# Kernel tuning notes

Measured on AMD Instinct MI355X. Metric: run time of the kernel, lower is better.

Reference implementation:

```python
import jax, jax.numpy as jnp
import numpy as np
import math

B, H, W, CV = 8, 128, 128, 256
T, CT = 77, 512
HEADS, HEAD_DIM = 8, 32
TOP_M = 5
LN_EPS = 1e-5
NORM_EPS = 1e-6
CLAMP = 2.0


def _ln(x, w, b):
    mu = jnp.mean(x, axis=-1, keepdims=True)
    var = jnp.mean(jnp.square(x - mu), axis=-1, keepdims=True)
    return (x - mu) * jax.lax.rsqrt(var + LN_EPS) * w + b


def _l2norm(x):
    n = jnp.sqrt(jnp.sum(jnp.square(x), axis=-1, keepdims=True))
    return x / jnp.maximum(n, NORM_EPS)


def setup_inputs() -> dict:
    key = jax.random.key(0)
    ks = jax.random.split(key, 12)
    s = 0.02
    return {
        "visual_features": jax.random.normal(ks[0], (B, H, W, CV), jnp.float32),
        "text_features": jax.random.normal(ks[1], (B, T, CT), jnp.float32),
        "norm1_w": jnp.ones((CV,), jnp.float32),
        "norm1_b": jnp.zeros((CV,), jnp.float32),
        "q_w": s * jax.random.normal(ks[2], (CV, CV), jnp.float32),
        "q_b": jnp.zeros((CV,), jnp.float32),
        "k_w": s * jax.random.normal(ks[3], (CT, CV), jnp.float32),
        "k_b": jnp.zeros((CV,), jnp.float32),
        "v_w": s * jax.random.normal(ks[4], (CT, CV), jnp.float32),
        "v_b": jnp.zeros((CV,), jnp.float32),
        "out_w": s * jax.random.normal(ks[5], (CV, CV), jnp.float32),
        "out_b": jnp.zeros((CV,), jnp.float32),
        "gate_w": s * jax.random.normal(ks[6], (CV, 1), jnp.float32),
        "gate_b": jnp.zeros((1,), jnp.float32),
        "logit_scale": jnp.asarray(math.log(1.0 / 0.07), jnp.float32),
        "alpha": jnp.asarray(0.1, jnp.float32),
        "norm2_w": jnp.ones((CV,), jnp.float32),
        "norm2_b": jnp.zeros((CV,), jnp.float32),
        "ffn1_w": s * jax.random.normal(ks[7], (CV, 4 * CV), jnp.float32),
        "ffn1_b": jnp.zeros((4 * CV,), jnp.float32),
        "ffn2_w": s * jax.random.normal(ks[8], (4 * CV, CV), jnp.float32),
        "ffn2_b": jnp.zeros((CV,), jnp.float32),
    }


def reference(visual_features, text_features, norm1_w, norm1_b, q_w, q_b, k_w, k_b,
              v_w, v_b, out_w, out_b, gate_w, gate_b, logit_scale, alpha,
              norm2_w, norm2_b, ffn1_w, ffn1_b, ffn2_w, ffn2_b):
    b, h, w, cv = visual_features.shape
    n = h * w
    # Pre-LN then flatten spatial dims: (B, N, Cv)
    x = _ln(visual_features, norm1_w, norm1_b).reshape(b, n, cv)
    q_full = x @ q_w + q_b                      # (B, N, Cv)
    k_full = text_features @ k_w + k_b          # (B, T, Cv)
    v_full = text_features @ v_w + v_b          # (B, T, Cv)
    # padding mask: all-zero text tokens
    pad = jnp.sum(jnp.abs(text_features), axis=-1) <= 1e-6  # (B, T)
    # cosine-normalize over FULL Cv dim, then split heads
    q = _l2norm(q_full).reshape(b, n, HEADS, HEAD_DIM)
    k = _l2norm(k_full).reshape(b, -1, HEADS, HEAD_DIM)
    v = v_full.reshape(b, -1, HEADS, HEAD_DIM)
    scale = jnp.exp(jnp.clip(logit_scale, -CLAMP, CLAMP)) / jnp.sqrt(jnp.float32(HEAD_DIM))
    sim = jnp.einsum('bnhd,bthd->bnht', q, k) * scale  # (B, N, Hh, T)
    sim = jnp.where(pad[:, None, None, :], -jnp.inf, sim)
    # top-k pruning over text tokens (threshold at k-th value; ties measure-zero)
    topv = jax.lax.top_k(sim, TOP_M)[0]
    sim = jnp.where(sim >= topv[..., -1:], sim, -jnp.inf)
    attn = jax.nn.softmax(sim, axis=-1)
    aligned = jnp.einsum('bnht,bthd->bnhd', attn, v).reshape(b, n, cv)
    aligned = aligned @ out_w + out_b
    gate = jax.nn.sigmoid(x @ gate_w + gate_b)  # (B, N, 1)
    y = x + alpha * gate * aligned
    y = _ln(y, norm2_w, norm2_b)
    ffn = jax.nn.gelu(y @ ffn1_w + ffn1_b, approximate=False) @ ffn2_w + ffn2_b
    y = y + ffn
    return y.reshape(b, h, w, cv)
```

## Files before the change

### kernel.cpp

```cpp
#include <hip/hip_runtime.h>
#include <hip/hip_bf16.h>

typedef _Float16 h16;
typedef __attribute__((ext_vector_type(8))) _Float16 halfx8;
typedef __attribute__((ext_vector_type(4))) _Float16 halfx4;
typedef __attribute__((ext_vector_type(4))) float f32x4;

__device__ __forceinline__ void gload_lds16(const void* g, void* l) {
  __builtin_amdgcn_global_load_lds((const __attribute__((address_space(1))) unsigned int*)g,
                                   (__attribute__((address_space(3))) unsigned int*)l, 16, 0, 0);
}
__device__ __forceinline__ unsigned umax_(unsigned a, unsigned b) { return a > b ? a : b; }
__device__ __forceinline__ unsigned umin_(unsigned a, unsigned b) { return a < b ? a : b; }

__device__ __forceinline__ float fast_gelu(float v) {
  float x2 = v * v;
  float w_ = v * fmaf(x2, 0.0713548163f, 1.5957691216f);
  float e = __expf(w_);
  float r = 1.f / (1.f + e);
  return v * e * r;
}

__global__ __launch_bounds__(256) void conv_all_kernel(
    const float* __restrict__ qw, const float* __restrict__ ow,
    const float* __restrict__ f1w, const float* __restrict__ f2w,
    h16* __restrict__ qwT, h16* __restrict__ owT,
    h16* __restrict__ f1T, h16* __restrict__ f2T)
{
  int bid = blockIdx.x, tid = threadIdx.x;
  const float* in; h16* out; int logN, K, base;
  if (bid < 256)       { in = qw;  out = qwT; logN = 8;  K = 256;  base = 0; }
  else if (bid < 512)  { in = ow;  out = owT; logN = 8;  K = 256;  base = 256; }
  else if (bid < 1536) { in = f1w; out = f1T; logN = 10; K = 256;  base = 512; }
  else                 { in = f2w; out = f2T; logN = 8;  K = 1024; base = 1536; }
  int idx = (bid - base) * 256 + tid;
  int k = idx >> logN, n = idx & ((1 << logN) - 1);
  out[(size_t)n * K + k] = (h16)in[idx];
}

__global__ __launch_bounds__(256) void text_kv_kernel(const float* __restrict__ tf,
    const float* __restrict__ kw, const float* __restrict__ kb,
    const float* __restrict__ vw, const float* __restrict__ vb,
    const float* __restrict__ lsp,
    h16* __restrict__ ko, h16* __restrict__ vo, float* __restrict__ padf)
{
  __shared__ h16 st[4 * 512];
  __shared__ float kro[4 * 256];
  __shared__ float ssc[4];
  int bx = blockIdx.x, b = bx / 20, tg = bx % 20, t0 = tg * 4;
  int tid = threadIdx.x, lane = tid & 63, wid = tid >> 6;
  for (int i = tid; i < 4 * 512; i += 256) {
    int tl = i >> 9, j = i & 511, t = t0 + tl;
    float v = (t < 77) ? tf[((size_t)b * 77 + t) * 512 + j] : 0.f;
    st[i] = (h16)v;
  }
  __syncthreads();
  {
    int t = t0 + wid;
    float a = 0.f;
    #pragma unroll
    for (int j = 0; j < 8; j++) a += fabsf((float)st[wid * 512 + lane + j * 64]);
    #pragma unroll
    for (int o = 32; o; o >>= 1) a += __shfl_xor(a, o);
    if (lane == 0) padf[b * 80 + t] = (a <= 1e-6f) ? -1e30f : 0.f;
  }
  int c = tid;
  float kacc[4], vacc[4];
  #pragma unroll
  for (int tl = 0; tl < 4; tl++) { kacc[tl] = kb[c]; vacc[tl] = vb[c]; }
  for (int j = 0; j < 512; j++) {
    float wkv = kw[(size_t)j * 256 + c];
    float wvv = vw[(size_t)j * 256 + c];
    #pragma unroll
    for (int tl = 0; tl < 4; tl++) {
      float x = (float)st[tl * 512 + j];
      kacc[tl] += x * wkv; vacc[tl] += x * wvv;
    }
  }
  #pragma unroll
  for (int tl = 0; tl < 4; tl++) kro[tl * 256 + c] = kacc[tl] * kacc[tl];
  __syncthreads();
  {
    float s2 = kro[wid * 256 + lane] + kro[wid * 256 + lane + 64]
             + kro[wid * 256 + lane + 128] + kro[wid * 256 + lane + 192];
    #pragma unroll
    for (int o = 32; o; o >>= 1) s2 += __shfl_xor(s2, o);
    if (lane == 0) {
      float ls = lsp[0];
      float scale = __expf(fminf(fmaxf(ls, -2.f), 2.f)) * rsqrtf(32.f);
      ssc[wid] = scale / fmaxf(sqrtf(s2), 1e-6f);
    }
  }
  __syncthreads();
  int h = c >> 5, d = c & 31, g = d >> 3, e = d & 7;
  #pragma unroll
  for (int tl = 0; tl < 4; tl++) {
    int t = t0 + tl;
    int kt = t >> 4, l15 = t & 15, ln = g * 16 + l15;
    size_t koff = ((((size_t)(b * 8 + h) * 5 + kt) * 64) + ln) * 8 + e;
    size_t voff = (((size_t)(b * 8 + h) * 80) + t) * 32 + d;
    ko[koff] = (t < 77) ? (h16)(kacc[tl] * ssc[tl]) : (h16)0.f;
    vo[voff] = (t < 77) ? (h16)vacc[tl] : (h16)0.f;
  }
}

__global__ __launch_bounds__(256) void ln1_kernel(const float* __restrict__ vis,
    const float* __restrict__ w, const float* __restrict__ bia,
    const float* __restrict__ gw, const float* __restrict__ gb,
    h16* __restrict__ x, float* __restrict__ gate)
{
  int lane = threadIdx.x & 63;
  size_t row = (size_t)blockIdx.x * 4 + (threadIdx.x >> 6);
  const float4 v = ((const float4*)(vis + row * 256))[lane];
  float s = v.x + v.y + v.z + v.w;
  float q = v.x * v.x + v.y * v.y + v.z * v.z + v.w * v.w;
  #pragma unroll
  for (int o = 32; o; o >>= 1) { s += __shfl_xor(s, o); q += __shfl_xor(q, o); }
  float mean = s * (1.f / 256.f);
  float rstd = rsqrtf(q * (1.f / 256.f) - mean * mean + 1e-5f);
  float4 wv = ((const float4*)w)[lane], bv = ((const float4*)bia)[lane];
  float x0 = (v.x - mean) * rstd * wv.x + bv.x;
  float x1 = (v.y - mean) * rstd * wv.y + bv.y;
  float x2 = (v.z - mean) * rstd * wv.z + bv.z;
  float x3 = (v.w - mean) * rstd * wv.w + bv.w;
  float4 gv = ((const float4*)gw)[lane];
  float g = x0 * gv.x + x1 * gv.y + x2 * gv.z + x3 * gv.w;
  #pragma unroll
  for (int o = 32; o; o >>= 1) g += __shfl_xor(g, o);
  if (lane == 0) gate[row] = 1.f / (1.f + __expf(-(g + gb[0])));
  halfx4 o4; o4[0] = (h16)x0; o4[1] = (h16)x1; o4[2] = (h16)x2; o4[3] = (h16)x3;
  ((halfx4*)(x + row * 256))[lane] = o4;
}

__global__ __launch_bounds__(256) void gemmQ_kernel(const h16* __restrict__ A,
    const h16* __restrict__ Wt, const float* __restrict__ bias, h16* __restrict__ outp)
{
  __shared__ char sA[8192];
  __shared__ char sB[32768];
  int m0 = blockIdx.x * 64;
  int tid = threadIdx.x, lane = tid & 63, wid = tid >> 6;
  int wn = wid;
  int l15 = lane & 15, l4 = lane >> 4, xk = l15 & 7;
  f32x4 acc[4][4];
  #pragma unroll
  for (int a = 0; a < 4; a++)
    #pragma unroll
    for (int b2 = 0; b2 < 4; b2++) acc[a][b2] = (f32x4){0.f, 0.f, 0.f, 0.f};
  const size_t sa = 512;
  int srow = lane >> 3;
  int scol = ((lane & 7) ^ srow) * 16;
  const char* Ab = (const char*)A + (size_t)m0 * sa + scol;
  const char* Bb = (const char*)Wt + scol;
  for (int k0 = 0; k0 < 256; k0 += 64) {
    #pragma unroll
    for (int cc = 0; cc < 2; cc++) {
      int ch = wid * 2 + cc;
      gload_lds16(Ab + (size_t)(ch * 8 + srow) * sa + k0 * 2, sA + ch * 1024);
    }
    #pragma unroll
    for (int cc = 0; cc < 8; cc++) {
      int ch = wid * 8 + cc;
      gload_lds16(Bb + (size_t)(ch * 8 + srow) * sa + k0 * 2, sB + ch * 1024);
    }
    asm volatile("s_waitcnt vmcnt(0)" ::: "memory");
    __syncthreads();
    #pragma unroll
    for (int ks = 0; ks < 2; ks++) {
      halfx8 af[4], bf[4];
      #pragma unroll
      for (int f = 0; f < 4; f++) {
        af[f] = *(const halfx8*)(sA + (f * 16 + l15) * 128 + (((ks * 4 + l4) ^ xk) * 16));
        bf[f] = *(const halfx8*)(sB + (wn * 64 + f * 16 + l15) * 128 + (((ks * 4 + l4) ^ xk) * 16));
      }
      #pragma unroll
      for (int fm = 0; fm < 4; fm++)
        #pragma unroll
        for (int fn = 0; fn < 4; fn++)
          acc[fm][fn] = __builtin_amdgcn_mfma_f32_16x16x32_f16(af[fm], bf[fn], acc[fm][fn], 0, 0, 0);
    }
    __syncthreads();
  }
  float bv[4];
  #pragma unroll
  for (int fn = 0; fn < 4; fn++) bv[fn] = bias[wn * 64 + fn * 16 + l15];
  float ps[4][4];
  #pragma unroll
  for (int fm = 0; fm < 4; fm++)
    #pragma unroll
    for (int r = 0; r < 4; r++) {
      float s = 0.f;
      #pragma unroll
      for (int fn = 0; fn < 4; fn++) {
        float v = acc[fm][fn][r] + bv[fn];
        acc[fm][fn][r] = v;
        s += v * v;
      }
      ps[fm][r] = s;
    }
  #pragma unroll
  for (int o = 1; o <= 8; o <<= 1)
    #pragma unroll
    for (int fm = 0; fm < 4; fm++)
      #pragma unroll
      for (int r = 0; r < 4; r++) ps[fm][r] += __shfl_xor(ps[fm][r], o);
  if (l15 == 0) {
    #pragma unroll
    for (int fm = 0; fm < 4; fm++)
      #pragma unroll
      for (int r = 0; r < 4; r++)
        ((float*)sA)[(fm * 16 + l4 * 4 + r) * 4 + wn] = ps[fm][r];
  }
  __syncthreads();
  #pragma unroll
  for (int fm = 0; fm < 4; fm++)
    #pragma unroll
    for (int r = 0; r < 4; r++) {
      const float* p = (const float*)sA + (fm * 16 + l4 * 4 + r) * 4;
      float S = p[0] + p[1] + p[2] + p[3];
      float sc = 1.f / fmaxf(sqrtf(S), 1e-6f);
      size_t row = (size_t)(m0 + fm * 16 + l4 * 4 + r);
      #pragma unroll
      for (int fn = 0; fn < 4; fn++)
        outp[row * 256 + wn * 64 + fn * 16 + l15] = (h16)(acc[fm][fn][r] * sc);
    }
}

__global__ __launch_bounds__(256) void gemmO_kernel(const h16* __restrict__ A,
    const h16* __restrict__ Wt, const float* __restrict__ ob,
    const h16* __restrict__ x, const float* __restrict__ gate,
    const float* __restrict__ alphap, const float* __restrict__ w2,
    const float* __restrict__ b2, h16* __restrict__ outp)
{
  __shared__ char sA[8192];
  __shared__ char sB[32768];
  int m0 = blockIdx.x * 64;
  int tid = threadIdx.x, lane = tid & 63, wid = tid >> 6;
  int wn = wid;
  int l15 = lane & 15, l4 = lane >> 4, xk = l15 & 7;
  f32x4 acc[4][4];
  #pragma unroll
  for (int a = 0; a < 4; a++)
    #pragma unroll
    for (int b2_ = 0; b2_ < 4; b2_++) acc[a][b2_] = (f32x4){0.f, 0.f, 0.f, 0.f};
  const size_t sa = 512;
  int srow = lane >> 3;
  int scol = ((lane & 7) ^ srow) * 16;
  const char* Ab = (const char*)A + (size_t)m0 * sa + scol;
  const char* Bb = (const char*)Wt + scol;
  for (int k0 = 0; k0 < 256; k0 += 64) {
    #pragma unroll
    for (int cc = 0; cc < 2; cc++) {
      int ch = wid * 2 + cc;
      gload_lds16(Ab + (size_t)(ch * 8 + srow) * sa + k0 * 2, sA + ch * 1024);
    }
    #pragma unroll
    for (int cc = 0; cc < 8; cc++) {
      int ch = wid * 8 + cc;
      gload_lds16(Bb + (size_t)(ch * 8 + srow) * sa + k0 * 2, sB + ch * 1024);
    }
    asm volatile("s_waitcnt vmcnt(0)" ::: "memory");
    __syncthreads();
    #pragma unroll
    for (int ks = 0; ks < 2; ks++) {
      halfx8 af[4], bf[4];
      #pragma unroll
      for (int f = 0; f < 4; f++) {
        af[f] = *(const halfx8*)(sA + (f * 16 + l15) * 128 + (((ks * 4 + l4) ^ xk) * 16));
        bf[f] = *(const halfx8*)(sB + (wn * 64 + f * 16 + l15) * 128 + (((ks * 4 + l4) ^ xk) * 16));
      }
      #pragma unroll
      for (int fm = 0; fm < 4; fm++)
        #pragma unroll
        for (int fn = 0; fn < 4; fn++)
          acc[fm][fn] = __builtin_amdgcn_mfma_f32_16x16x32_f16(af[fm], bf[fn], acc[fm][fn], 0, 0, 0);
    }
    __syncthreads();
  }
  float bv[4], w2v[4], b2v[4];
  #pragma unroll
  for (int fn = 0; fn < 4; fn++) {
    int col = wn * 64 + fn * 16 + l15;
    bv[fn] = ob[col]; w2v[fn] = w2[col]; b2v[fn] = b2[col];
  }
  float al = alphap[0];
  float s1[4][4], s2[4][4];
  #pragma unroll
  for (int fm = 0; fm < 4; fm++)
    #pragma unroll
    for (int r = 0; r < 4; r++) {
      size_t row = (size_t)(m0 + fm * 16 + l4 * 4 + r);
      float ga = al * gate[row];
      float a1 = 0.f, a2 = 0.f;
      #pragma unroll
      for (int fn = 0; fn < 4; fn++) {
        float v = acc[fm][fn][r] + bv[fn];
        float xv = (float)x[row * 256 + wn * 64 + fn * 16 + l15];
        float y = xv + ga * v;
        acc[fm][fn][r] = y;
        a1 += y; a2 += y * y;
      }
      s1[fm][r] = a1; s2[fm][r] = a2;
    }
  #pragma unroll
  for (int o = 1; o <= 8; o <<= 1)
    #pragma unroll
    for (int fm = 0; fm < 4; fm++)
      #pragma unroll
      for (int r = 0; r < 4; r++) {
        s1[fm][r] += __shfl_xor(s1[fm][r], o);
        s2[fm][r] += __shfl_xor(s2[fm][r], o);
      }
  if (l15 == 0) {
    #pragma unroll
    for (int fm = 0; fm < 4; fm++)
      #pragma unroll
      for (int r = 0; r < 4; r++) {
        int rr = fm * 16 + l4 * 4 + r;
        ((float*)sA)[rr * 8 + wn * 2 + 0] = s1[fm][r];
        ((float*)sA)[rr * 8 + wn * 2 + 1] = s2[fm][r];
      }
  }
  __syncthreads();
  #pragma unroll
  for (int fm = 0; fm < 4; fm++)
    #pragma unroll
    for (int r = 0; r < 4; r++) {
      int rr = fm * 16 + l4 * 4 + r;
      const float* p = (const float*)sA + rr * 8;
      float S1 = p[0] + p[2] + p[4] + p[6];
      float S2 = p[1] + p[3] + p[5] + p[7];
      float mean = S1 * (1.f / 256.f);
      float var = S2 * (1.f / 256.f) - mean * mean;
      float rstd = rsqrtf(var + 1e-5f);
      size_t row = (size_t)(m0 + rr);
      #pragma unroll
      for (int fn = 0; fn < 4; fn++) {
        float y = acc[fm][fn][r];
        outp[row * 256 + wn * 64 + fn * 16 + l15] =
            (h16)((y - mean) * rstd * w2v[fn] + b2v[fn]);
      }
    }
}

__device__ __forceinline__ void ffn_stage(const h16* __restrict__ w1t,
                                          const h16* __restrict__ w2t,
                                          int c, char* dW1, char* dW2, int tid, int wid)
{
  #pragma unroll
  for (int j = 0; j < 4; j++) {
    int i = j * 512 + tid;
    int r = i >> 5, g = i & 31;
    gload_lds16(w1t + (size_t)(c * 64 + r) * 256 + ((g ^ (r & 7)) * 8),
                dW1 + (j * 512 + wid * 64) * 16);
  }
  #pragma unroll
  for (int j = 0; j < 4; j++) {
    int i = j * 512 + tid;
    int r = i >> 3, g = i & 7;
    gload_lds16(w2t + (size_t)r * 1024 + c * 64 + ((g ^ (r & 7)) * 8),
                dW2 + (j * 512 + wid * 64) * 16);
  }
}

__global__ __launch_bounds__(512, 2) void ffn_fused_kernel(
    const h16* __restrict__ y2g, const h16* __restrict__ w1t, const float* __restrict__ b1,
    const h16* __restrict__ w2t, const float* __restrict__ b2, float* __restrict__ outp)
{
  __shared__ char smem[151552];
  char* sH = smem + 131072;
  float* sB1 = (float*)(smem + 147456);
  float* sE = (float*)smem;

  int m0 = blockIdx.x * 128;
  int tid = threadIdx.x, lane = tid & 63, wid = tid >> 6;
  int l15 = lane & 15, l4 = lane >> 4;
  int wm1 = wid >> 1, wn1 = wid & 1;
  int wm2 = wid >> 2, wn2 = wid & 3;

  ((float2*)sB1)[tid] = ((const float2*)b1)[tid];

  halfx8 afy[2][8];
  #pragma unroll
  for (int fm = 0; fm < 2; fm++) {
    size_t row = (size_t)(m0 + wm1 * 32 + fm * 16 + l15);
    #pragma unroll
    for (int ks = 0; ks < 8; ks++)
      afy[fm][ks] = *(const halfx8*)&y2g[row * 256 + ks * 32 + l4 * 8];
  }

  f32x4 acc2[4][4];
  #pragma unroll
  for (int a = 0; a < 4; a++)
    #pragma unroll
    for (int b_ = 0; b_ < 4; b_++) acc2[a][b_] = (f32x4){0.f, 0.f, 0.f, 0.f};

  ffn_stage(w1t, w2t, 0, smem, smem + 65536, tid, wid);
  asm volatile("s_waitcnt lgkmcnt(0)" ::: "memory");

  for (int c = 0; c < 16; c++) {
    int buf = c & 1;
    char* sW1 = smem + buf * 32768;
    char* sW2 = smem + 65536 + buf * 32768;
    if (c < 15) {
      ffn_stage(w1t, w2t, c + 1, smem + (buf ^ 1) * 32768,
                smem + 65536 + (buf ^ 1) * 32768, tid, wid);
      asm volatile("s_waitcnt vmcnt(8)" ::: "memory");
    } else {
      asm volatile("s_waitcnt vmcnt(0)" ::: "memory");
    }
    __builtin_amdgcn_s_barrier();
    asm volatile("" ::: "memory");

    float b1v0 = sB1[c * 64 + wn1 * 32 + l15];
    float b1v1 = sB1[c * 64 + wn1 * 32 + 16 + l15];

    f32x4 a1[2][2];
    #pragma unroll
    for (int a = 0; a < 2; a++)
      #pragma unroll
      for (int b_ = 0; b_ < 2; b_++) a1[a][b_] = (f32x4){0.f, 0.f, 0.f, 0.f};
    __builtin_amdgcn_s_setprio(1);
    #pragma unroll
    for (int ks = 0; ks < 8; ks++) {
      #pragma unroll
      for (int fc = 0; fc < 2; fc++) {
        int nrow = wn1 * 32 + fc * 16 + l15;
        halfx8 bf = *(const halfx8*)(sW1 + (size_t)nrow * 512 + (((ks * 4 + l4) ^ (nrow & 7)) * 16));
        #pragma unroll
        for (int fm = 0; fm < 2; fm++)
          a1[fm][fc] = __builtin_amdgcn_mfma_f32_16x16x32_f16(afy[fm][ks], bf, a1[fm][fc], 0, 0, 0);
      }
    }
    __builtin_amdgcn_s_setprio(0);
    #pragma unroll
    for (int fm = 0; fm < 2; fm++)
      #pragma unroll
      for (int fc = 0; fc < 2; fc++)
        #pragma unroll
        for (int r = 0; r < 4; r++) {
          int row = wm1 * 32 + fm * 16 + l4 * 4 + r;
          int col = wn1 * 32 + fc * 16 + l15;
          float v = fast_gelu(a1[fm][fc][r] + (fc ? b1v1 : b1v0));
          ((h16*)(sH + row * 128 + (((col >> 3) ^ (row & 7)) * 16)))[col & 7] = (h16)v;
        }
    asm volatile("s_waitcnt lgkmcnt(0)" ::: "memory");
    __builtin_amdgcn_s_barrier();
    asm volatile("" ::: "memory");
    __builtin_amdgcn_s_setprio(1);
    #pragma unroll
    for (int ks = 0; ks < 2; ks++) {
      halfx8 ah[4], bw[4];
      #pragma unroll
      for (int f = 0; f < 4; f++) {
        int hrow = wm2 * 64 + f * 16 + l15;
        ah[f] = *(const halfx8*)(sH + hrow * 128 + (((ks * 4 + l4) ^ (hrow & 7)) * 16));
        int wrow = wn2 * 64 + f * 16 + l15;
        bw[f] = *(const halfx8*)(sW2 + (size_t)wrow * 128 + (((ks * 4 + l4) ^ (wrow & 7)) * 16));
      }
      #pragma unroll
      for (int fm = 0; fm < 4; fm++)
        #pragma unroll
        for (int fn = 0; fn < 4; fn++)
          acc2[fm][fn] = __builtin_amdgcn_mfma_f32_16x16x32_f16(ah[fm], bw[fn], acc2[fm][fn], 0, 0, 0);
    }
    __builtin_amdgcn_s_setprio(0);
    asm volatile("" ::: "memory");
    __builtin_amdgcn_s_barrier();
    asm volatile("" ::: "memory");
  }

  int rowl = tid >> 3, cg = tid & 7;
  #pragma unroll
  for (int half = 0; half < 2; half++) {
    if (wm2 == half) {
      #pragma unroll
      for (int fm = 0; fm < 4; fm++)
        #pragma unroll
        for (int fn = 0; fn < 4; fn++)
          #pragma unroll
          for (int r = 0; r < 4; r++)
            sE[(fm * 16 + l4 * 4 + r) * 264 + wn2 * 64 + fn * 16 + l15] = acc2[fm][fn][r];
    }
    __syncthreads();
    size_t grow = (size_t)(m0 + half * 64 + rowl);
    #pragma unroll
    for (int k = 0; k < 8; k++) {
      int c0 = cg * 4 + k * 32;
      float4 v = *(float4*)&sE[rowl * 264 + c0];
      halfx4 rv = *(const halfx4*)&y2g[grow * 256 + c0];
      float4 bb = *(const float4*)&b2[c0];
      float4 o;
      o.x = v.x + (float)rv[0] + bb.x;
      o.y = v.y + (float)rv[1] + bb.y;
      o.z = v.z + (float)rv[2] + bb.z;
      o.w = v.w + (float)rv[3] + bb.w;
      *(float4*)&outp[grow * 256 + c0] = o;
    }
    __syncthreads();
  }
}

__global__ __launch_bounds__(256) void attn_kernel(const h16* __restrict__ q,
    const h16* __restrict__ kk,
    const h16* __restrict__ vv,
    const float* __restrict__ padf,
    h16* __restrict__ outp)
{
  int bx = blockIdx.x;
  int wid = threadIdx.x >> 6, lane = threadIdx.x & 63;
  int l15 = lane & 15, g = lane >> 4;
  int b = bx >> 8;
  size_t qrow = (size_t)bx * 64 + wid * 16 + l15;
  int base4 = g * 4;
  float pad4[5][4];
  #pragma unroll
  for (int kt = 0; kt < 5; kt++) {
    float4 p4 = *(const float4*)&padf[b * 80 + kt * 16 + base4];
    pad4[kt][0] = p4.x; pad4[kt][1] = p4.y; pad4[kt][2] = p4.z; pad4[kt][3] = p4.w;
  }
  const h16* qp = &q[qrow * 256 + g * 8];
  h16* op = &outp[qrow * 256 + g * 8];
  #pragma unroll 2
  for (int h = 0; h < 8; h++) {
    int ho = h * 32;
    halfx8 qf = *(const halfx8*)(qp + ho);
    const h16* kph = kk + (((size_t)(b * 8 + h) * 5) * 64 + lane) * 8;
    const h16* vph = vv + ((size_t)(b * 8 + h) * 80) * 32 + g * 8;
    f32x4 acc[5];
    #pragma unroll
    for (int kt = 0; kt < 5; kt++) {
      halfx8 kf = *(const halfx8*)(kph + kt * 512);
      acc[kt] = __builtin_amdgcn_mfma_f32_16x16x32_f16(kf, qf, (f32x4){0.f, 0.f, 0.f, 0.f}, 0, 0, 0);
    }
    unsigned pv0 = 0u, pv1 = 0u, pv2 = 0u, pv3 = 0u, pv4 = 0u;
    #pragma unroll
    for (int kt = 0; kt < 5; kt++) {
      #pragma unroll
      for (int r = 0; r < 4; r++) {
        float s = acc[kt][r] + pad4[kt][r];
        int bi = __float_as_int(s);
        unsigned u = ((unsigned)(bi ^ ((bi >> 31) | (int)0x80000000)) & 0xFFFFFF80u)
                   | (unsigned)(base4 + kt * 16 + r);
        unsigned a;
        a = umax_(pv0, u); u = umin_(pv0, u); pv0 = a;
        a = umax_(pv1, u); u = umin_(pv1, u); pv1 = a;
        a = umax_(pv2, u); u = umin_(pv2, u); pv2 = a;
        a = umax_(pv3, u); u = umin_(pv3, u); pv3 = a;
        pv4 = umax_(pv4, u);
      }
    }
    #pragma unroll
    for (int mrd = 0; mrd < 2; mrd++) {
      int msk = mrd ? 32 : 16;
      unsigned b0 = (unsigned)__shfl_xor((int)pv0, msk);
      unsigned b1 = (unsigned)__shfl_xor((int)pv1, msk);
      unsigned b2 = (unsigned)__shfl_xor((int)pv2, msk);
      unsigned b3 = (unsigned)__shfl_xor((int)pv3, msk);
      unsigned b4 = (unsigned)__shfl_xor((int)pv4, msk);
      unsigned c0 = umax_(pv0, b0);
      unsigned c1 = umax_(umax_(umin_(pv0, b0), pv1), b1);
      unsigned c2 = umax_(umax_(umin_(pv0, b1), umin_(pv1, b0)), umax_(pv2, b2));
      unsigned c3 = umax_(umax_(umax_(umin_(pv0, b2), umin_(pv1, b1)), umin_(pv2, b0)), umax_(pv3, b3));
      unsigned c4 = umax_(umax_(umax_(umin_(pv0, b3), umin_(pv1, b2)),
                                umax_(umin_(pv2, b1), umin_(pv3, b0))), umax_(pv4, b4));
      pv0 = c0; pv1 = c1; pv2 = c2; pv3 = c3; pv4 = c4;
    }
    unsigned pvs[5] = {pv0, pv1, pv2, pv3, pv4};
    float pw[5]; int ti[5]; float den = 0.f;
    #pragma unroll
    for (int k = 0; k < 5; k++) {
      unsigned u = pvs[k];
      int sg = ((int)u) >> 31;
      float tv = __int_as_float(u ^ (0x80000000u | (unsigned)~sg));
      ti[k] = (int)(u & 0x7Fu);
      pw[k] = __expf(tv);
      den += pw[k];
    }
    float inv = 1.f / den;
    halfx8 o8 = {};
    #pragma unroll
    for (int k = 0; k < 5; k++) {
      h16 ph = (h16)(pw[k] * inv);
      halfx8 v = *(const halfx8*)(vph + ti[k] * 32);
      halfx8 p8 = {ph, ph, ph, ph, ph, ph, ph, ph};
      o8 = o8 + p8 * v;
    }
    *(halfx8*)(op + ho) = o8;
  }
}

extern "C" void kernel_launch(void* const* d_in, const int* in_sizes, int n_in,
                              void* d_out, int out_size, void* d_ws, size_t ws_size,
                              hipStream_t stream)
{
  const float* vis = (const float*)d_in[0];
  const float* tf  = (const float*)d_in[1];
  const float* n1w = (const float*)d_in[2];
  const float* n1b = (const float*)d_in[3];
  const float* qw  = (const float*)d_in[4];
  const float* qb  = (const float*)d_in[5];
  const float* kw  = (const float*)d_in[6];
  const float* kb  = (const float*)d_in[7];
  const float* vw  = (const float*)d_in[8];
  const float* vb  = (const float*)d_in[9];
  const float* ow  = (const float*)d_in[10];
  const float* ob  = (const float*)d_in[11];
  const float* gw  = (const float*)d_in[12];
  const float* gb  = (const float*)d_in[13];
  const float* ls  = (const float*)d_in[14];
  const float* al  = (const float*)d_in[15];
  const float* n2w = (const float*)d_in[16];
  const float* n2b = (const float*)d_in[17];
  const float* f1w = (const float*)d_in[18];
  const float* f1b = (const float*)d_in[19];
  const float* f2w = (const float*)d_in[20];
  const float* f2b = (const float*)d_in[21];

  char* ws = (char*)d_ws;
  const size_t MB_ = 1024ull * 1024ull;
  h16*  kS   = (h16*)(ws + 0 * MB_);
  h16*  vS   = (h16*)(ws + 1 * MB_);
  float* padf = (float*)(ws + 2 * MB_);
  float* gate = (float*)(ws + 3 * MB_);
  h16*  qwT  = (h16*)(ws + 4 * MB_);
  h16*  owT  = (h16*)(ws + 5 * MB_);
  h16*  f1T  = (h16*)(ws + 6 * MB_);
  h16*  f2T  = (h16*)(ws + 7 * MB_);
  h16*  xh   = (h16*)(ws + 16 * MB_);
  h16*  qh   = (h16*)(ws + 80 * MB_);
  h16*  alg  = (h16*)(ws + 144 * MB_);

  conv_all_kernel<<<2560, 256, 0, stream>>>(qw, ow, f1w, f2w, qwT, owT, f1T, f2T);

  text_kv_kernel<<<160, 256, 0, stream>>>(tf, kw, kb, vw, vb, ls, kS, vS, padf);
  ln1_kernel<<<32768, 256, 0, stream>>>(vis, n1w, n1b, gw, gb, xh, gate);

  gemmQ_kernel<<<2048, 256, 0, stream>>>(xh, qwT, qb, qh);

  attn_kernel<<<2048, 256, 0, stream>>>(qh, kS, vS, padf, qh);

  gemmO_kernel<<<2048, 256, 0, stream>>>(qh, owT, ob, xh, gate, al, n2w, n2b, alg);

  ffn_fused_kernel<<<1024, 512, 0, stream>>>(alg, f1T, f1b, f2T, f2b, (float*)d_out);
}
```

Measured before the change: 550.9 us.

## Software-pipeline FFN: overlap GEMM1 of chunk c with GEMM2 of chunk c-1

Restructures the fused FFN loop so that each iteration computes the first GEMM plus GELU for chunk c into a double-buffered hidden tile, then runs the second GEMM for chunk c-1. This removes one of the two barriers per iteration and lets the two MFMA phases interleave. It also loads the W2 chunk one iteration later and reads bias values straight from global memory into registers instead of staging them in LDS. LDS use grows to hold two hidden buffers, and every iteration now waits for all outstanding global loads before its barrier.

```diff
diff --git a/kernel.cpp b/kernel.cpp
--- a/kernel.cpp
+++ b/kernel.cpp
@@ -342,9 +342,8 @@
     }
 }
 
-__device__ __forceinline__ void ffn_stage(const h16* __restrict__ w1t,
-                                          const h16* __restrict__ w2t,
-                                          int c, char* dW1, char* dW2, int tid, int wid)
+__device__ __forceinline__ void ffn_stage_w1(const h16* __restrict__ w1t,
+                                             int c, char* dW1, int tid, int wid)
 {
   #pragma unroll
   for (int j = 0; j < 4; j++) {
@@ -353,6 +352,10 @@
     gload_lds16(w1t + (size_t)(c * 64 + r) * 256 + ((g ^ (r & 7)) * 8),
                 dW1 + (j * 512 + wid * 64) * 16);
   }
+}
+__device__ __forceinline__ void ffn_stage_w2(const h16* __restrict__ w2t,
+                                             int c, char* dW2, int tid, int wid)
+{
   #pragma unroll
   for (int j = 0; j < 4; j++) {
     int i = j * 512 + tid;
@@ -366,9 +369,7 @@
     const h16* __restrict__ y2g, const h16* __restrict__ w1t, const float* __restrict__ b1,
     const h16* __restrict__ w2t, const float* __restrict__ b2, float* __restrict__ outp)
 {
-  __shared__ char smem[151552];
-  char* sH = smem + 131072;
-  float* sB1 = (float*)(smem + 147456);
+  __shared__ char smem[163840];
   float* sE = (float*)smem;
 
   int m0 = blockIdx.x * 128;
@@ -377,8 +378,6 @@
   int wm1 = wid >> 1, wn1 = wid & 1;
   int wm2 = wid >> 2, wn2 = wid & 3;
 
-  ((float2*)sB1)[tid] = ((const float2*)b1)[tid];
-
   halfx8 afy[2][8];
   #pragma unroll
   for (int fm = 0; fm < 2; fm++) {
@@ -394,58 +393,91 @@
     #pragma unroll
     for (int b_ = 0; b_ < 4; b_++) acc2[a][b_] = (f32x4){0.f, 0.f, 0.f, 0.f};
 
-  ffn_stage(w1t, w2t, 0, smem, smem + 65536, tid, wid);
-  asm volatile("s_waitcnt lgkmcnt(0)" ::: "memory");
+  ffn_stage_w1(w1t, 0, smem, tid, wid);
+  float b1v0 = b1[wn1 * 32 + l15];
+  float b1v1 = b1[wn1 * 32 + 16 + l15];
+  asm volatile("s_waitcnt vmcnt(0)" ::: "memory");
+  __builtin_amdgcn_s_barrier();
+  asm volatile("" ::: "memory");
 
   for (int c = 0; c < 16; c++) {
     int buf = c & 1;
-    char* sW1 = smem + buf * 32768;
-    char* sW2 = smem + 65536 + buf * 32768;
+    char* sW1c = smem + buf * 32768;
+    if (c < 15) ffn_stage_w1(w1t, c + 1, smem + (buf ^ 1) * 32768, tid, wid);
+    ffn_stage_w2(w2t, c, smem + 65536 + buf * 32768, tid, wid);
+    float nb0 = 0.f, nb1 = 0.f;
     if (c < 15) {
-      ffn_stage(w1t, w2t, c + 1, smem + (buf ^ 1) * 32768,
-                smem + 65536 + (buf ^ 1) * 32768, tid, wid);
-      asm volatile("s_waitcnt vmcnt(8)" ::: "memory");
-    } else {
-      asm volatile("s_waitcnt vmcnt(0)" ::: "memory");
-    }
+      nb0 = b1[(c + 1) * 64 + wn1 * 32 + l15];
+      nb1 = b1[(c + 1) * 64 + wn1 * 32 + 16 + l15];
+    }
+
+    f32x4 a1[2][2];
+    #pragma unroll
+    for (int a = 0; a < 2; a++)
+      #pragma unroll
+      for (int b_ = 0; b_ < 2; b_++) a1[a][b_] = (f32x4){0.f, 0.f, 0.f, 0.f};
+    __builtin_amdgcn_s_setprio(1);
+    #pragma unroll
+    for (int ks = 0; ks < 8; ks++) {
+      #pragma unroll
+      for (int fc = 0; fc < 2; fc++) {
+        int nrow = wn1 * 32 + fc * 16 + l15;
+        halfx8 bf = *(const halfx8*)(sW1c + (size_t)nrow * 512 + (((ks * 4 + l4) ^ (nrow & 7)) * 16));
+        #pragma unroll
+        for (int fm = 0; fm < 2; fm++)
+          a1[fm][fc] = __builtin_amdgcn_mfma_f32_16x16x32_f16(afy[fm][ks], bf, a1[fm][fc], 0, 0, 0);
+      }
+    }
+    __builtin_amdgcn_s_setprio(0);
+
+    {
+      char* sHc = smem + 131072 + buf * 16384;
+      #pragma unroll
+      for (int fm = 0; fm < 2; fm++)
+        #pragma unroll
+        for (int fc = 0; fc < 2; fc++)
+          #pragma unroll
+          for (int r = 0; r < 4; r++) {
+            int row = wm1 * 32 + fm * 16 + l4 * 4 + r;
+            int col = wn1 * 32 + fc * 16 + l15;
+            float v = fast_gelu(a1[fm][fc][r] + (fc ? b1v1 : b1v0));
+            ((h16*)(sHc + row * 128 + (((col >> 3) ^ (row & 7)) * 16)))[col & 7] = (h16)v;
+          }
+    }
+
+    if (c > 0) {
+      char* sHp = smem + 131072 + (buf ^ 1) * 16384;
+      char* sW2p = smem + 65536 + (buf ^ 1) * 32768;
+      __builtin_amdgcn_s_setprio(1);
+      #pragma unroll
+      for (int ks = 0; ks < 2; ks++) {
+        halfx8 ah[4], bw[4];
+        #pragma unroll
+        for (int f = 0; f < 4; f++) {
+          int hrow = wm2 * 64 + f * 16 + l15;
+          ah[f] = *(const halfx8*)(sHp + hrow * 128 + (((ks * 4 + l4) ^ (hrow & 7)) * 16));
+          int wrow = wn2 * 64 + f * 16 + l15;
+          bw[f] = *(const halfx8*)(sW2p + (size_t)wrow * 128 + (((ks * 4 + l4) ^ (wrow & 7)) * 16));
+        }
+        #pragma unroll
+        for (int fm = 0; fm < 4; fm++)
+          #pragma unroll
+          for (int fn = 0; fn < 4; fn++)
+            acc2[fm][fn] = __builtin_amdgcn_mfma_f32_16x16x32_f16(ah[fm], bw[fn], acc2[fm][fn], 0, 0, 0);
+      }
+      __builtin_amdgcn_s_setprio(0);
+    }
+
+    asm volatile("s_waitcnt lgkmcnt(0)" ::: "memory");
+    asm volatile("s_waitcnt vmcnt(0)" ::: "memory");
     __builtin_amdgcn_s_barrier();
     asm volatile("" ::: "memory");
-
-    float b1v0 = sB1[c * 64 + wn1 * 32 + l15];
-    float b1v1 = sB1[c * 64 + wn1 * 32 + 16 + l15];
-
-    f32x4 a1[2][2];
-    #pragma unroll
-    for (int a = 0; a < 2; a++)
-      #pragma unroll
-      for (int b_ = 0; b_ < 2; b_++) a1[a][b_] = (f32x4){0.f, 0.f, 0.f, 0.f};
-    __builtin_amdgcn_s_setprio(1);
-    #pragma unroll
-    for (int ks = 0; ks < 8; ks++) {
-      #pragma unroll
-      for (int fc = 0; fc < 2; fc++) {
-        int nrow = wn1 * 32 + fc * 16 + l15;
-        halfx8 bf = *(const halfx8*)(sW1 + (size_t)nrow * 512 + (((ks * 4 + l4) ^ (nrow & 7)) * 16));
-        #pragma unroll
-        for (int fm = 0; fm < 2; fm++)
-          a1[fm][fc] = __builtin_amdgcn_mfma_f32_16x16x32_f16(afy[fm][ks], bf, a1[fm][fc], 0, 0, 0);
-      }
-    }
-    __builtin_amdgcn_s_setprio(0);
-    #pragma unroll
-    for (int fm = 0; fm < 2; fm++)
-      #pragma unroll
-      for (int fc = 0; fc < 2; fc++)
-        #pragma unroll
-        for (int r = 0; r < 4; r++) {
-          int row = wm1 * 32 + fm * 16 + l4 * 4 + r;
-          int col = wn1 * 32 + fc * 16 + l15;
-          float v = fast_gelu(a1[fm][fc][r] + (fc ? b1v1 : b1v0));
-          ((h16*)(sH + row * 128 + (((col >> 3) ^ (row & 7)) * 16)))[col & 7] = (h16)v;
-        }
-    asm volatile("s_waitcnt lgkmcnt(0)" ::: "memory");
-    __builtin_amdgcn_s_barrier();
-    asm volatile("" ::: "memory");
+    b1v0 = nb0; b1v1 = nb1;
+  }
+
+  {
+    char* sHp = smem + 131072 + 16384;
+    char* sW2p = smem + 65536 + 32768;
     __builtin_amdgcn_s_setprio(1);
     #pragma unroll
     for (int ks = 0; ks < 2; ks++) {
@@ -453,9 +485,9 @@
       #pragma unroll
       for (int f = 0; f < 4; f++) {
         int hrow = wm2 * 64 + f * 16 + l15;
-        ah[f] = *(const halfx8*)(sH + hrow * 128 + (((ks * 4 + l4) ^ (hrow & 7)) * 16));
+        ah[f] = *(const halfx8*)(sHp + hrow * 128 + (((ks * 4 + l4) ^ (hrow & 7)) * 16));
         int wrow = wn2 * 64 + f * 16 + l15;
-        bw[f] = *(const halfx8*)(sW2 + (size_t)wrow * 128 + (((ks * 4 + l4) ^ (wrow & 7)) * 16));
+        bw[f] = *(const halfx8*)(sW2p + (size_t)wrow * 128 + (((ks * 4 + l4) ^ (wrow & 7)) * 16));
       }
       #pragma unroll
       for (int fm = 0; fm < 4; fm++)
@@ -464,9 +496,6 @@
           acc2[fm][fn] = __builtin_amdgcn_mfma_f32_16x16x32_f16(ah[fm], bw[fn], acc2[fm][fn], 0, 0, 0);
     }
     __builtin_amdgcn_s_setprio(0);
-    asm volatile("" ::: "memory");
-    __builtin_amdgcn_s_barrier();
-    asm volatile("" ::: "memory");
   }
 
   int rowl = tid >> 3, cg = tid & 7;
```

Result: no change. 544.3 us (-1.2%).
